# Optimization experiments

Measured on AMD Instinct MI355X. Metric: run time of the kernel, lower is better.

## Reference

```python
import jax, jax.numpy as jnp
import numpy as np

SIGMA = 4.0
KSIZE = 2 * int(4.0 * SIGMA + 0.5) + 1  # 33, as in anomalib's GaussianBlur2d
INPUT_SIZE = (224, 224)
NUM_NEIGHBORS = 9


def avg_pool_4_1_1(x):
    # nn.AvgPool2d(kernel_size=4, stride=1, padding=1), count_include_pad=True -> divide by 16
    s = jax.lax.reduce_window(x, 0.0, jax.lax.add, (1, 1, 4, 4), (1, 1, 1, 1),
                              ((0, 0), (0, 0), (1, 1), (1, 1)))
    return s / 16.0


def gaussian_kernel1d(ksize, sigma):
    x = jnp.arange(ksize, dtype=jnp.float32) - (ksize - 1) / 2.0
    g = jnp.exp(-0.5 * (x / sigma) ** 2)
    return g / jnp.sum(g)


def gaussian_blur(x):
    # separable 33x33 gaussian blur, reflect padding (kornia GaussianBlur2d default)
    k = gaussian_kernel1d(KSIZE, SIGMA)
    pad = KSIZE // 2
    xp = jnp.pad(x, ((0, 0), (0, 0), (pad, pad), (pad, pad)), mode='reflect')
    dn = ('NCHW', 'OIHW', 'NCHW')
    y = jax.lax.conv_general_dilated(xp, k.reshape(1, 1, KSIZE, 1), (1, 1), 'VALID', dimension_numbers=dn)
    y = jax.lax.conv_general_dilated(y, k.reshape(1, 1, 1, KSIZE), (1, 1), 'VALID', dimension_numbers=dn)
    return y


def euclidean_dist(x, y):
    # pairwise L2: x [..., n, d], y [..., m, d] -> [..., n, m]
    x2 = jnp.sum(x * x, axis=-1, keepdims=True)
    y2 = jnp.sum(y * y, axis=-1, keepdims=True)
    d2 = x2 - 2.0 * jnp.matmul(x, jnp.swapaxes(y, -1, -2)) + jnp.swapaxes(y2, -1, -2)
    return jnp.sqrt(jnp.clip(d2, 0.0, None))


def compute_anomaly_score(patch_scores, locations, embedding, memory_bank):
    # PatchCore re-weighting (num_neighbors > 1 branch)
    B, P = patch_scores.shape
    bidx = jnp.arange(B)
    max_patches = jnp.argmax(patch_scores, axis=1)                      # [B]
    feats = embedding.reshape(B, P, -1)[bidx, max_patches]              # [B, C]
    score = patch_scores[bidx, max_patches]                             # [B] s*
    nn_index = locations[bidx, max_patches]                             # [B]
    nn_sample = memory_bank[nn_index]                                   # [B, C]
    d_bank = euclidean_dist(nn_sample, memory_bank)                     # [B, M]
    _, support = jax.lax.top_k(-d_bank, NUM_NEIGHBORS)                  # [B, K] smallest
    support_feats = memory_bank[support]                                # [B, K, C]
    distances = euclidean_dist(feats[:, None, :], support_feats)        # [B, 1, K]
    weights = 1.0 - jnp.exp(score) / jnp.sum(jnp.exp(distances[:, 0, :]), axis=-1)
    return weights * score


def setup_inputs() -> dict:
    key = jax.random.key(0)
    k1, k2, k3 = jax.random.split(key, 3)
    feat_layer2 = jax.random.normal(k1, (8, 512, 28, 28), dtype=jnp.float32)
    feat_layer3 = jax.random.normal(k2, (8, 1024, 14, 14), dtype=jnp.float32)
    memory_bank = jax.random.normal(k3, (32000, 1536), dtype=jnp.float32)
    return {"feat_layer2": feat_layer2, "feat_layer3": feat_layer3, "memory_bank": memory_bank}


def reference(feat_layer2, feat_layer3, memory_bank):
    # feature_pooler = AvgPool2d(4,1,1)
    f2 = avg_pool_4_1_1(feat_layer2)   # [B, 512, 27, 27]
    f3 = avg_pool_4_1_1(feat_layer3)   # [B, 1024, 13, 13]
    B, _, H, W = f2.shape
    # generate_embedding: bilinear upsample layer3 to layer2 size, concat channels
    f3u = jax.image.resize(f3, (B, f3.shape[1], H, W), method='bilinear')
    emb = jnp.concatenate([f2, f3u], axis=1)                            # [B, 1536, 27, 27]
    C = emb.shape[1]
    embedding = jnp.transpose(emb, (0, 2, 3, 1)).reshape(-1, C)         # [B*H*W, C]
    # nearest_neighbors with n_neighbors=1 over the coreset memory bank
    d = euclidean_dist(embedding, memory_bank)                          # [B*H*W, M]
    patch_scores = jnp.min(d, axis=1).reshape(B, -1)
    locations = jnp.argmin(d, axis=1).reshape(B, -1)
    pred_score = compute_anomaly_score(patch_scores, locations, embedding, memory_bank)
    # anomaly map: upsample patch scores to input size + gaussian blur
    pmap = patch_scores.reshape(B, 1, H, W)
    amap = jax.image.resize(pmap, (B, 1, INPUT_SIZE[0], INPUT_SIZE[1]), method='bilinear')
    anomaly_map = gaussian_blur(amap)
    return anomaly_map, pred_score
```

## Files before the change

kernel.cpp:

```cpp
#include <hip/hip_runtime.h>
#include <math.h>

#define NB 8
#define C2 512
#define C3 1024
#define HIN2 28
#define HIN3 14
#define HO2 27
#define HO3 13
#define CC 1536
#define NP (NB*HO2*HO2)
#define NM 32000
#define NKNN 9
#define OH 224
#define AMAP_N (NB*OH*OH)

#define BM 256
#define BN 256
#define BK 64
#define KT (CC/BK)
#define MB_CNT ((NP+BM-1)/BM)
#define NB_CNT (NM/BN)
#define NWG (MB_CNT*NB_CNT)

typedef unsigned long long u64;
typedef unsigned int u32;
typedef __attribute__((ext_vector_type(8))) short bf16x8;
typedef __attribute__((ext_vector_type(4))) float f32x4;

struct GW { float w[33]; };

__device__ __forceinline__ float warp_sum(float v){
  #pragma unroll
  for (int off=32; off; off>>=1) v += __shfl_down(v, off);
  return v;
}

__device__ __forceinline__ ushort f2bf(float f){
  u32 u = __float_as_uint(f);
  u32 r = (u + 0x7FFFu + ((u>>16)&1u)) >> 16;
  return (ushort)r;
}
__device__ __forceinline__ float bf2f(ushort b){
  return __uint_as_float(((u32)b)<<16);
}

#define GLDS(g, l) __builtin_amdgcn_global_load_lds((const __attribute__((address_space(1))) void*)(g), (__attribute__((address_space(3))) void*)(l), 16, 0, 0)
#define WAITVM4() asm volatile("s_waitcnt vmcnt(4)" ::: "memory")
#define WAITVM0() asm volatile("s_waitcnt vmcnt(0)" ::: "memory")
#define WAITLGKM0() asm volatile("s_waitcnt lgkmcnt(0)" ::: "memory")
#define SB0() __builtin_amdgcn_sched_barrier(0)
__device__ __forceinline__ void bar_raw(){
  asm volatile("" ::: "memory");
  __builtin_amdgcn_s_barrier();
  asm volatile("" ::: "memory");
}

__global__ __launch_bounds__(256) void k_avgpool2(const float* __restrict__ in, ushort* __restrict__ embB){
  __shared__ float pl[16*789];
  int b = blockIdx.x >> 5, cg = blockIdx.x & 31;
  const float4* src = (const float4*)(in + ((size_t)b*C2 + cg*16)*(HIN2*HIN2));
  for (int idx = threadIdx.x; idx < 16*196; idx += 256){
    int c = idx/196, p4 = idx - c*196;
    float4 v = src[idx];
    float* d = &pl[c*789 + p4*4];
    d[0]=v.x; d[1]=v.y; d[2]=v.z; d[3]=v.w;
  }
  __syncthreads();
  int c = threadIdx.x & 15, g = threadIdx.x >> 4;
  for (int pos = g; pos < HO2*HO2; pos += 16){
    int i = pos/HO2, j = pos - i*HO2;
    const float* p = &pl[c*789];
    float s = 0.f;
    #pragma unroll
    for (int di=0; di<4; ++di){
      int y = i - 1 + di;
      if ((unsigned)y >= HIN2) continue;
      #pragma unroll
      for (int dj=0; dj<4; ++dj){
        int x = j - 1 + dj;
        if ((unsigned)x < HIN2) s += p[y*HIN2 + x];
      }
    }
    embB[((size_t)((b*HO2 + i)*HO2 + j))*CC + cg*16 + c] = f2bf(s * (1.f/16.f));
  }
}

__global__ __launch_bounds__(256) void k_avgpool3(const float* __restrict__ in, float* __restrict__ f3p){
  __shared__ float pl[64*197];
  int b = blockIdx.x >> 4, cg = blockIdx.x & 15;
  const float4* src = (const float4*)(in + ((size_t)b*C3 + cg*64)*(HIN3*HIN3));
  for (int idx = threadIdx.x; idx < 64*49; idx += 256){
    int c = idx/49, p4 = idx - c*49;
    float4 v = src[idx];
    float* d = &pl[c*197 + p4*4];
    d[0]=v.x; d[1]=v.y; d[2]=v.z; d[3]=v.w;
  }
  __syncthreads();
  int c = threadIdx.x & 63, g = threadIdx.x >> 6;
  for (int pos = g; pos < HO3*HO3; pos += 4){
    int i = pos/HO3, j = pos - i*HO3;
    const float* p = &pl[c*197];
    float s = 0.f;
    #pragma unroll
    for (int di=0; di<4; ++di){
      int y = i - 1 + di;
      if ((unsigned)y >= HIN3) continue;
      #pragma unroll
      for (int dj=0; dj<4; ++dj){
        int x = j - 1 + dj;
        if ((unsigned)x < HIN3) s += p[y*HIN3 + x];
      }
    }
    f3p[((size_t)((b*HO3 + i)*HO3 + j))*C3 + cg*64 + c] = s * (1.f/16.f);
  }
}

__global__ void k_upsample3(const float* __restrict__ f3p, ushort* __restrict__ embB){
  int t = blockIdx.x*256 + threadIdx.x;
  if (t >= NB*HO2*HO2*C3) return;
  int c = t % C3; int r = t / C3;
  int ox = r % HO2; r /= HO2;
  int oy = r % HO2; int b = r / HO2;
  float fy = (oy + 0.5f) * (13.f/27.f) - 0.5f;
  float fx = (ox + 0.5f) * (13.f/27.f) - 0.5f;
  int y0 = (int)floorf(fy); float wy = fy - (float)y0;
  int x0 = (int)floorf(fx); float wx = fx - (float)x0;
  int y0c = min(max(y0,0), HO3-1), y1c = min(max(y0+1,0), HO3-1);
  int x0c = min(max(x0,0), HO3-1), x1c = min(max(x0+1,0), HO3-1);
  const float* base = f3p + (size_t)(b*HO3*HO3)*C3;
  float v00 = base[(size_t)(y0c*HO3 + x0c)*C3 + c];
  float v01 = base[(size_t)(y0c*HO3 + x1c)*C3 + c];
  float v10 = base[(size_t)(y1c*HO3 + x0c)*C3 + c];
  float v11 = base[(size_t)(y1c*HO3 + x1c)*C3 + c];
  float v = (1.f-wy)*((1.f-wx)*v00 + wx*v01) + wy*((1.f-wx)*v10 + wx*v11);
  embB[((size_t)((b*HO2 + oy)*HO2 + ox))*CC + C2 + c] = f2bf(v);
}

__global__ void k_bank_prep(const float* __restrict__ bank, ushort* __restrict__ bankB,
                            float* __restrict__ y2){
  int wave = threadIdx.x >> 6, lane = threadIdx.x & 63;
  int r = blockIdx.x*4 + wave;
  if (r >= NM) return;
  const float4* p = (const float4*)(bank + (size_t)r*CC);
  ushort4* q = (ushort4*)(bankB + (size_t)r*CC);
  float s = 0.f;
  #pragma unroll
  for (int it=0; it<6; ++it){
    float4 v = p[it*64 + lane];
    s += v.x*v.x + v.y*v.y + v.z*v.z + v.w*v.w;
    ushort4 o; o.x = f2bf(v.x); o.y = f2bf(v.y); o.z = f2bf(v.z); o.w = f2bf(v.w);
    q[it*64 + lane] = o;
  }
  s = warp_sum(s);
  if (lane==0) y2[r] = s;
}

__global__ void k_rowsumsq_bf(const ushort* __restrict__ src, float* __restrict__ dst, int rows,
                              u64* __restrict__ packed){
  int wave = threadIdx.x >> 6;
  int lane = threadIdx.x & 63;
  int r = blockIdx.x*4 + wave;
  if (r >= rows) return;
  const uint4* p = (const uint4*)(src + (size_t)r*CC);
  float s = 0.f;
  #pragma unroll
  for (int it=0; it<3; ++it){
    uint4 v = p[it*64 + lane];
    u32 ws_[4] = {v.x, v.y, v.z, v.w};
    #pragma unroll
    for (int q=0;q<4;q++){
      float lo = __uint_as_float(ws_[q]<<16);
      float hi = __uint_as_float(ws_[q]&0xFFFF0000u);
      s += lo*lo + hi*hi;
    }
  }
  s = warp_sum(s);
  if (lane==0){ dst[r] = s; packed[r] = ~0ull; }
}

__global__ __launch_bounds__(512, 2) void k_distmin_mfma(
    const ushort* __restrict__ A, const ushort* __restrict__ B,
    const float* __restrict__ x2, const float* __restrict__ y2,
    u64* __restrict__ packed)
{
  __shared__ ushort smem[4*BM*BK];
  ushort* As0 = smem;
  ushort* Bs0 = smem + BM*BK;
  ushort* As1 = smem + 2*BM*BK;
  ushort* Bs1 = smem + 3*BM*BK;

  const int tid = threadIdx.x;
  const int w   = tid >> 6;
  const int l   = tid & 63;
  const int wr  = w >> 2;
  const int wc  = w & 3;
  const int ccol = l & 15;
  const int cgrp = l >> 4;

  int orig = blockIdx.x;
  const int q8 = NWG/8, r8 = NWG%8;
  int xcd = orig & 7, sidx = orig >> 3;
  int wg = (xcd < r8 ? xcd*(q8+1) : r8*(q8+1) + (xcd-r8)*q8) + sidx;
  const int mb = wg % MB_CNT;
  const int nb = wg / MB_CNT;
  const int m0 = mb * BM;
  const int n0 = nb * BN;

  const int rowin = l >> 3;
  const int scol  = (((l&7) ^ rowin) * 8);
  int chA1[2], chA2[2], chB1[2], chB2[2];
  u32 aO1[2], aO2[2], bO1[2], bO2[2];
  u32 lA1[2], lA2[2], lB1[2], lB2[2];
  #pragma unroll
  for (int c=0;c<2;c++){
    chA1[c] = (w<4) ? (2*w+c) : (8+2*w+c);
    chA2[c] = chA1[c] + 8;
    chB1[c] = (w>>1)*8 + (w&1)*2 + c;
    chB2[c] = chB1[c] + 4;
    aO1[c] = (u32)min(m0 + chA1[c]*8 + rowin, NP-1)*CC + scol;
    aO2[c] = (u32)min(m0 + chA2[c]*8 + rowin, NP-1)*CC + scol;
    bO1[c] = (u32)(n0 + chB1[c]*8 + rowin)*CC + scol;
    bO2[c] = (u32)(n0 + chB2[c]*8 + rowin)*CC + scol;
    lA1[c] = (u32)chA1[c]*1024 + l*16;
    lA2[c] = (u32)chA2[c]*1024 + l*16;
    lB1[c] = (u32)chB1[c]*1024 + l*16;
    lB2[c] = (u32)chB2[c]*1024 + l*16;
  }

  const u32 o0 = (u32)((cgrp ^ (ccol & 7)) * 8);
  u32 aRow[8], bRow[4];
  #pragma unroll
  for (int mi=0;mi<8;mi++) aRow[mi] = (u32)(wr*128 + mi*16 + ccol)*BK;
  #pragma unroll
  for (int ni=0;ni<4;ni++) bRow[ni] = (u32)(wc*64 + ni*16 + ccol)*BK;

  f32x4 acc[8][4];
  #pragma unroll
  for (int mi=0;mi<8;mi++)
    #pragma unroll
    for (int ni=0;ni<4;ni++)
      acc[mi][ni] = (f32x4){0.f,0.f,0.f,0.f};

  bf16x8 rAlo[4][2], rAhi[4][2], rBlo[2][2], rBhi[2][2];

  GLDS(A + aO1[0], (char*)As0 + lA1[0]);
  GLDS(A + aO1[1], (char*)As0 + lA1[1]);
  GLDS(B + bO1[0], (char*)Bs0 + lB1[0]);
  GLDS(B + bO1[1], (char*)Bs0 + lB1[1]);
  GLDS(B + bO2[0], (char*)Bs0 + lB2[0]);
  GLDS(B + bO2[1], (char*)Bs0 + lB2[1]);
  GLDS(A + aO2[0], (char*)As0 + lA2[0]);
  GLDS(A + aO2[1], (char*)As0 + lA2[1]);
  WAITVM4();
  bar_raw();

  const ushort* cA = As0; const ushort* cB = Bs0;
  ushort* nA = As1; ushort* nB = Bs1;

  #pragma unroll 1
  for (int kt=0; kt<KT; ++kt){
    const u32 kk = (u32)(kt+1)*BK;

    #pragma unroll
    for (int mi=0;mi<4;mi++)
      #pragma unroll
      for (int ks=0;ks<2;ks++)
        rAlo[mi][ks] = *(const bf16x8*)&cA[aRow[mi] + (o0 ^ (u32)(ks<<5))];
    #pragma unroll
    for (int ni=0;ni<2;ni++)
      #pragma unroll
      for (int ks=0;ks<2;ks++)
        rBlo[ni][ks] = *(const bf16x8*)&cB[bRow[ni] + (o0 ^ (u32)(ks<<5))];
    GLDS(A + aO1[0] + kk, (char*)nA + lA1[0]);
    GLDS(A + aO1[1] + kk, (char*)nA + lA1[1]);
    bar_raw(); WAITLGKM0(); SB0();
    __builtin_amdgcn_s_setprio(1);
    #pragma unroll
    for (int mi=0;mi<4;mi++)
      #pragma unroll
      for (int ni=0;ni<2;ni++)
        #pragma unroll
        for (int ks=0;ks<2;ks++)
          acc[mi][ni] = __builtin_amdgcn_mfma_f32_16x16x32_bf16(rAlo[mi][ks], rBlo[ni][ks], acc[mi][ni], 0, 0, 0);
    __builtin_amdgcn_s_setprio(0);
    WAITVM4();
    bar_raw();

    #pragma unroll
    for (int ni=0;ni<2;ni++)
      #pragma unroll
      for (int ks=0;ks<2;ks++)
        rBhi[ni][ks] = *(const bf16x8*)&cB[bRow[ni+2] + (o0 ^ (u32)(ks<<5))];
    GLDS(B + bO1[0] + kk, (char*)nB + lB1[0]);
    GLDS(B + bO1[1] + kk, (char*)nB + lB1[1]);
    bar_raw(); WAITLGKM0(); SB0();
    __builtin_amdgcn_s_setprio(1);
    #pragma unroll
    for (int mi=0;mi<4;mi++)
      #pragma unroll
      for (int ni=0;ni<2;ni++)
        #pragma unroll
        for (int ks=0;ks<2;ks++)
          acc[mi][ni+2] = __builtin_amdgcn_mfma_f32_16x16x32_bf16(rAlo[mi][ks], rBhi[ni][ks], acc[mi][ni+2], 0, 0, 0);
    __builtin_amdgcn_s_setprio(0);
    WAITVM4();
    bar_raw();

    #pragma unroll
    for (int mi=0;mi<4;mi++)
      #pragma unroll
      for (int ks=0;ks<2;ks++)
        rAhi[mi][ks] = *(const bf16x8*)&cA[aRow[mi+4] + (o0 ^ (u32)(ks<<5))];
    GLDS(B + bO2[0] + kk, (char*)nB + lB2[0]);
    GLDS(B + bO2[1] + kk, (char*)nB + lB2[1]);
    bar_raw(); WAITLGKM0(); SB0();
    __builtin_amdgcn_s_setprio(1);
    #pragma unroll
    for (int mi=0;mi<4;mi++)
      #pragma unroll
      for (int ni=0;ni<2;ni++)
        #pragma unroll
        for (int ks=0;ks<2;ks++)
          acc[mi+4][ni] = __builtin_amdgcn_mfma_f32_16x16x32_bf16(rAhi[mi][ks], rBlo[ni][ks], acc[mi+4][ni], 0, 0, 0);
    __builtin_amdgcn_s_setprio(0);
    bar_raw();

    GLDS(A + aO2[0] + kk, (char*)nA + lA2[0]);
    GLDS(A + aO2[1] + kk, (char*)nA + lA2[1]);
    bar_raw();
    __builtin_amdgcn_s_setprio(1);
    #pragma unroll
    for (int mi=0;mi<4;mi++)
      #pragma unroll
      for (int ni=0;ni<2;ni++)
        #pragma unroll
        for (int ks=0;ks<2;ks++)
          acc[mi+4][ni+2] = __builtin_amdgcn_mfma_f32_16x16x32_bf16(rAhi[mi][ks], rBhi[ni][ks], acc[mi+4][ni+2], 0, 0, 0);
    __builtin_amdgcn_s_setprio(0);
    WAITVM4();
    bar_raw();

    ushort* t1 = (ushort*)cA; cA = nA; nA = t1;
    ushort* t2 = (ushort*)cB; cB = nB; nB = t2;
  }
  WAITVM0();

  float xv[8][4];
  #pragma unroll
  for (int mi=0;mi<8;mi++)
    #pragma unroll
    for (int r=0;r<4;r++)
      xv[mi][r] = x2[min(m0 + wr*128 + mi*16 + cgrp*4 + r, NP-1)];

  u64 best[8][4];
  #pragma unroll
  for (int mi=0;mi<8;mi++)
    #pragma unroll
    for (int r=0;r<4;r++) best[mi][r] = ~0ull;

  #pragma unroll
  for (int ni=0;ni<4;ni++){
    const int n = n0 + wc*64 + ni*16 + ccol;
    const float yy = y2[n];
    #pragma unroll
    for (int mi=0;mi<8;mi++)
      #pragma unroll
      for (int r=0;r<4;r++){
        float d2 = fmaxf(xv[mi][r] + yy - 2.f*acc[mi][ni][r], 0.f);
        u64 pk = (((u64)__float_as_uint(d2))<<32) | (u32)n;
        if (pk < best[mi][r]) best[mi][r] = pk;
      }
  }

  #pragma unroll
  for (int mi=0;mi<8;mi++)
    #pragma unroll
    for (int r=0;r<4;r++){
      u64 pk = best[mi][r];
      #pragma unroll
      for (int md=1; md<16; md<<=1){
        u64 o = __shfl_xor(pk, md);
        if (o < pk) pk = o;
      }
      const int row = m0 + wr*128 + mi*16 + cgrp*4 + r;
      if (ccol==0 && row < NP) atomicMin(&packed[row], pk);
    }
}

__global__ void k_unpack(const u64* __restrict__ packed, float* __restrict__ patch_d, int* __restrict__ loc){
  int t = blockIdx.x*256 + threadIdx.x;
  if (t < NP){
    u64 v = packed[t];
    patch_d[t] = sqrtf(__uint_as_float((u32)(v>>32)));
    loc[t] = (int)(v & 0xffffffffu);
  }
}

__global__ void k_argmax(const float* __restrict__ patch_d, const int* __restrict__ loc,
                         int* __restrict__ sel_mp, float* __restrict__ sel_score, int* __restrict__ sel_nn){
  int b = blockIdx.x;
  int tid = threadIdx.x;
  __shared__ u64 red[4];
  u64 best = 0;
  for (int p = tid; p < HO2*HO2; p += 256){
    float v = patch_d[b*HO2*HO2 + p];
    u64 pk = (((u64)__float_as_uint(v))<<32) | (u32)(HO2*HO2 - p);
    if (pk > best) best = pk;
  }
  int lane = tid & 63, w = tid >> 6;
  #pragma unroll
  for (int d=32; d; d>>=1){ u64 o = __shfl_down(best, d); if (o > best) best = o; }
  if (lane==0) red[w] = best;
  __syncthreads();
  if (tid==0){
    u64 bb = red[0];
    for (int q=1;q<4;q++) if (red[q] > bb) bb = red[q];
    int p = HO2*HO2 - (int)(bb & 0xffffffffu);
    sel_mp[b] = p;
    sel_score[b] = __uint_as_float((u32)(bb>>32));
    sel_nn[b] = loc[b*HO2*HO2 + p];
  }
}

__device__ __forceinline__ void bf8dec(uint4 v, float* f){
  u32 a[4] = {v.x, v.y, v.z, v.w};
  #pragma unroll
  for (int q=0;q<4;q++){
    f[2*q]   = __uint_as_float(a[q]<<16);
    f[2*q+1] = __uint_as_float(a[q]&0xFFFF0000u);
  }
}

__global__ __launch_bounds__(256) void k_dbank(const ushort* __restrict__ bankB, const float* __restrict__ y2,
    const int* __restrict__ sel_nn, float* __restrict__ d_bank){
  int wave = threadIdx.x >> 6, lane = threadIdx.x & 63;
  int m = blockIdx.x*4 + wave;
  if (m >= NM) return;
  int nn[NB];
  #pragma unroll
  for (int b=0;b<NB;b++) nn[b] = sel_nn[b];
  const uint4* pm = (const uint4*)(bankB + (size_t)m*CC);
  float acc[NB];
  #pragma unroll
  for (int b=0;b<NB;b++) acc[b] = 0.f;
  #pragma unroll
  for (int it=0; it<3; ++it){
    uint4 v = pm[it*64 + lane];
    float vf[8]; bf8dec(v, vf);
    #pragma unroll
    for (int b=0;b<NB;b++){
      uint4 u = ((const uint4*)(bankB + (size_t)nn[b]*CC))[it*64 + lane];
      float uf[8]; bf8dec(u, uf);
      #pragma unroll
      for (int q=0;q<8;q++) acc[b] += vf[q]*uf[q];
    }
  }
  #pragma unroll
  for (int b=0;b<NB;b++){
    float s = warp_sum(acc[b]);
    if (lane==0) d_bank[(size_t)b*NM + m] = fmaxf(y2[nn[b]] + y2[m] - 2.f*s, 0.f);
  }
}

__global__ __launch_bounds__(512) void k_score(const float* __restrict__ d_bank, const float* __restrict__ bank,
    const ushort* __restrict__ embB, const float* __restrict__ x2, const float* __restrict__ y2,
    const int* __restrict__ sel_mp, const float* __restrict__ sel_score, float* __restrict__ out_score){
  int b = blockIdx.x, tid = threadIdx.x;
  __shared__ u64 cand[512*NKNN];
  __shared__ int sel[NKNN];
  __shared__ u64 red[8];
  __shared__ u64 gbest_s;
  __shared__ float fred[8];
  __shared__ float sumexp_s;

  #pragma unroll
  for (int q=0;q<NKNN;q++) cand[tid*NKNN+q] = ~0ull;
  for (int m = tid; m < NM; m += 512){
    float v = d_bank[(size_t)b*NM + m];
    u64 pk = (((u64)__float_as_uint(v))<<32) | (u32)m;
    if (pk < cand[tid*NKNN + NKNN-1]){
      cand[tid*NKNN + NKNN-1] = pk;
      for (int q=NKNN-1; q>0 && cand[tid*NKNN+q] < cand[tid*NKNN+q-1]; --q){
        u64 t = cand[tid*NKNN+q]; cand[tid*NKNN+q] = cand[tid*NKNN+q-1]; cand[tid*NKNN+q-1] = t;
      }
    }
  }
  __syncthreads();
  int lane = tid & 63, w = tid >> 6;
  for (int k=0;k<NKNN;++k){
    u64 mybest = ~0ull;
    #pragma unroll
    for (int q=0;q<NKNN;q++){ u64 v = cand[tid*NKNN+q]; if (v < mybest) mybest = v; }
    u64 rb = mybest;
    #pragma unroll
    for (int d=32; d; d>>=1){ u64 o = __shfl_down(rb, d); if (o < rb) rb = o; }
    if (lane==0) red[w] = rb;
    __syncthreads();
    if (tid==0){
      u64 bb = red[0];
      for (int q=1;q<8;q++) if (red[q] < bb) bb = red[q];
      gbest_s = bb;
      sel[k] = (int)(bb & 0xffffffffu);
    }
    __syncthreads();
    u64 gb = gbest_s;
    #pragma unroll
    for (int q=0;q<NKNN;q++) if (cand[tid*NKNN+q] == gb) cand[tid*NKNN+q] = ~0ull;
    __syncthreads();
  }

  int mp = sel_mp[b];
  const ushort* fv = embB + (size_t)(b*HO2*HO2 + mp)*CC;
  float fx2 = x2[b*HO2*HO2 + mp];
  if (tid==0) sumexp_s = 0.f;
  __syncthreads();
  for (int k=0;k<NKNN;++k){
    const float* sv = bank + (size_t)sel[k]*CC;
    float part = 0.f;
    for (int i = tid; i < CC; i += 512) part += bf2f(fv[i])*sv[i];
    part = warp_sum(part);
    if (lane==0) fred[w] = part;
    __syncthreads();
    if (tid==0){
      float dot = 0.f;
      for (int q=0;q<8;q++) dot += fred[q];
      float d2 = fmaxf(fx2 + y2[sel[k]] - 2.f*dot, 0.f);
      sumexp_s += expf(sqrtf(d2));
    }
    __syncthreads();
  }
  if (tid==0){
    float s = sel_score[b];
    out_score[b] = (1.f - expf(s)/sumexp_s) * s;
  }
}

__global__ void k_maketab(float* __restrict__ T, GW gw){
  int idx = blockIdx.x*256 + threadIdx.x;
  if (idx >= OH*HO2) return;
  int x = idx / HO2, j = idx - x*HO2;
  float s = 0.f;
  #pragma unroll
  for (int k=0;k<33;++k){
    int yy = x + k - 16;
    yy = (yy < 0) ? -yy : yy;
    yy = (yy > OH-1) ? (2*(OH-1) - yy) : yy;
    float fy = (yy + 0.5f) * (27.f/224.f) - 0.5f;
    int y0 = (int)floorf(fy); float wy = fy - (float)y0;
    int j0 = min(max(y0,0), HO2-1), j1 = min(max(y0+1,0), HO2-1);
    float c = ((j==j0)?(1.f-wy):0.f) + ((j==j1)?wy:0.f);
    s += gw.w[k]*c;
  }
  T[idx] = s;
}

__global__ __launch_bounds__(256) void k_amap_fused(const float* __restrict__ patch_d,
    const float* __restrict__ T, float* __restrict__ out){
  __shared__ float Ts[OH*HO2];
  __shared__ float ps[HO2*HO2];
  __shared__ float tmp[HO2*OH];
  int b = blockIdx.x, t = threadIdx.x;
  for (int idx=t; idx<OH*HO2; idx+=256) Ts[idx] = T[idx];
  for (int idx=t; idx<HO2*HO2; idx+=256) ps[idx] = patch_d[b*HO2*HO2+idx];
  __syncthreads();
  for (int idx=t; idx<HO2*OH; idx+=256){
    int i = idx/OH, x = idx - i*OH;
    float s = 0.f;
    #pragma unroll
    for (int j=0;j<HO2;j++) s += ps[i*HO2+j]*Ts[x*HO2+j];
    tmp[i*OH+x] = s;
  }
  __syncthreads();
  for (int idx=t; idx<OH*OH; idx+=256){
    int y = idx/OH, x = idx - y*OH;
    float s = 0.f;
    #pragma unroll
    for (int i=0;i<HO2;i++) s += Ts[y*HO2+i]*tmp[i*OH+x];
    out[(size_t)b*OH*OH + idx] = s;
  }
}

extern "C" void kernel_launch(void* const* d_in, const int* in_sizes, int n_in,
                              void* d_out, int out_size, void* d_ws, size_t ws_size,
                              hipStream_t stream){
  const float* f2   = (const float*)d_in[0];
  const float* f3   = (const float*)d_in[1];
  const float* bank = (const float*)d_in[2];
  float* out = (float*)d_out;

  char* ws = (char*)d_ws;
  size_t off = 0;
  auto alloc = [&](size_t bytes)->char*{ char* p = ws + off; off += (bytes + 255) & ~(size_t)255; return p; };
  ushort* embB    = (ushort*)alloc((size_t)NP*CC*2);
  ushort* bankB   = (ushort*)alloc((size_t)NM*CC*2);
  float* f3p      = (float*)alloc((size_t)NB*HO3*HO3*C3*4);
  float* y2       = (float*)alloc((size_t)NM*4);
  float* x2       = (float*)alloc((size_t)NP*4);
  u64*   packed   = (u64*)  alloc((size_t)NP*8);
  float* patch_d  = (float*)alloc((size_t)NP*4);
  int*   loc      = (int*)  alloc((size_t)NP*4);
  float* d_bank   = (float*)alloc((size_t)NB*NM*4);
  int*   sel_mp   = (int*)  alloc(NB*4);
  float* sel_scr  = (float*)alloc(NB*4);
  int*   sel_nn   = (int*)  alloc(NB*4);
  float* Tmat     = (float*)alloc((size_t)OH*HO2*4);

  GW gw;
  { float s=0.f; for(int i=0;i<33;i++){ float xx=(float)i-16.f; gw.w[i]=expf(-0.5f*(xx/4.f)*(xx/4.f)); s+=gw.w[i]; }
    for(int i=0;i<33;i++) gw.w[i]/=s; }

  k_avgpool2<<<NB*32,256,0,stream>>>(f2, embB);
  k_avgpool3<<<NB*16,256,0,stream>>>(f3, f3p);
  k_upsample3<<<(NB*HO2*HO2*C3+255)/256,256,0,stream>>>(f3p, embB);
  k_bank_prep<<<(NM+3)/4,256,0,stream>>>(bank, bankB, y2);
  k_rowsumsq_bf<<<(NP+3)/4,256,0,stream>>>(embB, x2, NP, packed);
  k_maketab<<<(OH*HO2+255)/256,256,0,stream>>>(Tmat, gw);
  k_distmin_mfma<<<NWG,512,0,stream>>>(embB, bankB, x2, y2, packed);
  k_unpack<<<(NP+255)/256,256,0,stream>>>(packed, patch_d, loc);
  k_argmax<<<NB,256,0,stream>>>(patch_d, loc, sel_mp, sel_scr, sel_nn);
  k_dbank<<<(NM+3)/4,256,0,stream>>>(bankB, y2, sel_nn, d_bank);
  k_score<<<NB,512,0,stream>>>(d_bank, bank, embB, x2, y2, sel_mp, sel_scr, out + AMAP_N);
  k_amap_fused<<<NB,256,0,stream>>>(patch_d, Tmat, out);
}
```

Baseline: 949.6 us.

## Load A fragments directly from global into registers, keep B in LDS

The distance GEMM kernel stops staging the embedding (A) tile through LDS. Each wave now loads its A fragments straight from global memory into registers and prefetches the next K step between MFMA halves. Only the memory-bank (B) tile stays double-buffered in LDS, which halves LDS use and removes several barriers and lgkm waits per K step. The tile order also changes so the N index varies fastest. In exchange, the four column waves fetch the same A rows redundantly from cache with less coalesced per-lane 16-byte loads, and the prefetch on the final step reads past the end of K.

After: 1.784 ms. 1.88x slower.

```diff
diff --git a/kernel.cpp b/kernel.cpp
--- a/kernel.cpp
+++ b/kernel.cpp
@@ -46,9 +46,8 @@
 }
 
 #define GLDS(g, l) __builtin_amdgcn_global_load_lds((const __attribute__((address_space(1))) void*)(g), (__attribute__((address_space(3))) void*)(l), 16, 0, 0)
-#define WAITVM4() asm volatile("s_waitcnt vmcnt(4)" ::: "memory")
+#define WAITVM16() asm volatile("s_waitcnt vmcnt(16)" ::: "memory")
 #define WAITVM0() asm volatile("s_waitcnt vmcnt(0)" ::: "memory")
-#define WAITLGKM0() asm volatile("s_waitcnt lgkmcnt(0)" ::: "memory")
 #define SB0() __builtin_amdgcn_sched_barrier(0)
 __device__ __forceinline__ void bar_raw(){
   asm volatile("" ::: "memory");
@@ -184,11 +183,9 @@
     const float* __restrict__ x2, const float* __restrict__ y2,
     u64* __restrict__ packed)
 {
-  __shared__ ushort smem[4*BM*BK];
-  ushort* As0 = smem;
-  ushort* Bs0 = smem + BM*BK;
-  ushort* As1 = smem + 2*BM*BK;
-  ushort* Bs1 = smem + 3*BM*BK;
+  __shared__ ushort smem[2*BN*BK];
+  ushort* Bs0 = smem;
+  ushort* Bs1 = smem + BN*BK;
 
   const int tid = threadIdx.x;
   const int w   = tid >> 6;
@@ -202,36 +199,28 @@
   const int q8 = NWG/8, r8 = NWG%8;
   int xcd = orig & 7, sidx = orig >> 3;
   int wg = (xcd < r8 ? xcd*(q8+1) : r8*(q8+1) + (xcd-r8)*q8) + sidx;
-  const int mb = wg % MB_CNT;
-  const int nb = wg / MB_CNT;
+  const int nb = wg % NB_CNT;
+  const int mb = wg / NB_CNT;
   const int m0 = mb * BM;
   const int n0 = nb * BN;
 
   const int rowin = l >> 3;
   const int scol  = (((l&7) ^ rowin) * 8);
-  int chA1[2], chA2[2], chB1[2], chB2[2];
-  u32 aO1[2], aO2[2], bO1[2], bO2[2];
-  u32 lA1[2], lA2[2], lB1[2], lB2[2];
-  #pragma unroll
-  for (int c=0;c<2;c++){
-    chA1[c] = (w<4) ? (2*w+c) : (8+2*w+c);
-    chA2[c] = chA1[c] + 8;
-    chB1[c] = (w>>1)*8 + (w&1)*2 + c;
-    chB2[c] = chB1[c] + 4;
-    aO1[c] = (u32)min(m0 + chA1[c]*8 + rowin, NP-1)*CC + scol;
-    aO2[c] = (u32)min(m0 + chA2[c]*8 + rowin, NP-1)*CC + scol;
-    bO1[c] = (u32)(n0 + chB1[c]*8 + rowin)*CC + scol;
-    bO2[c] = (u32)(n0 + chB2[c]*8 + rowin)*CC + scol;
-    lA1[c] = (u32)chA1[c]*1024 + l*16;
-    lA2[c] = (u32)chA2[c]*1024 + l*16;
-    lB1[c] = (u32)chB1[c]*1024 + l*16;
-    lB2[c] = (u32)chB2[c]*1024 + l*16;
-  }
+  u32 bOff[4]; u32 lOff[4];
+  #pragma unroll
+  for (int c=0;c<4;c++){
+    int chunk = w*4 + c;
+    bOff[c] = (u32)(n0 + chunk*8 + rowin)*CC + scol;
+    lOff[c] = (u32)chunk*1024 + l*16;
+  }
+
+  u32 aOff[8];
+  #pragma unroll
+  for (int mi=0;mi<8;mi++)
+    aOff[mi] = (u32)min(m0 + wr*128 + mi*16 + ccol, NP-1)*CC + cgrp*8;
 
   const u32 o0 = (u32)((cgrp ^ (ccol & 7)) * 8);
-  u32 aRow[8], bRow[4];
-  #pragma unroll
-  for (int mi=0;mi<8;mi++) aRow[mi] = (u32)(wr*128 + mi*16 + ccol)*BK;
+  u32 bRow[4];
   #pragma unroll
   for (int ni=0;ni<4;ni++) bRow[ni] = (u32)(wc*64 + ni*16 + ccol)*BK;
 
@@ -242,107 +231,72 @@
     for (int ni=0;ni<4;ni++)
       acc[mi][ni] = (f32x4){0.f,0.f,0.f,0.f};
 
-  bf16x8 rAlo[4][2], rAhi[4][2], rBlo[2][2], rBhi[2][2];
-
-  GLDS(A + aO1[0], (char*)As0 + lA1[0]);
-  GLDS(A + aO1[1], (char*)As0 + lA1[1]);
-  GLDS(B + bO1[0], (char*)Bs0 + lB1[0]);
-  GLDS(B + bO1[1], (char*)Bs0 + lB1[1]);
-  GLDS(B + bO2[0], (char*)Bs0 + lB2[0]);
-  GLDS(B + bO2[1], (char*)Bs0 + lB2[1]);
-  GLDS(A + aO2[0], (char*)As0 + lA2[0]);
-  GLDS(A + aO2[1], (char*)As0 + lA2[1]);
-  WAITVM4();
-  bar_raw();
-
-  const ushort* cA = As0; const ushort* cB = Bs0;
-  ushort* nA = As1; ushort* nB = Bs1;
+  bf16x8 aF[8][2], bF[4][2];
+
+  #pragma unroll
+  for (int c=0;c<4;c++) GLDS(B + bOff[c], (char*)Bs0 + lOff[c]);
+  #pragma unroll
+  for (int mi=0;mi<8;mi++)
+    #pragma unroll
+    for (int ks=0;ks<2;ks++)
+      aF[mi][ks] = *(const bf16x8*)(A + aOff[mi] + ks*32);
+  #pragma unroll
+  for (int mi=0;mi<8;mi++) aOff[mi] += 64;
+  WAITVM0(); bar_raw(); SB0();
+
+  const ushort* cB = Bs0; ushort* nB = Bs1;
 
   #pragma unroll 1
   for (int kt=0; kt<KT; ++kt){
-    const u32 kk = (u32)(kt+1)*BK;
-
+    #pragma unroll
+    for (int ni=0;ni<4;ni++)
+      #pragma unroll
+      for (int ks=0;ks<2;ks++)
+        bF[ni][ks] = *(const bf16x8*)&cB[bRow[ni] + (o0 ^ (u32)(ks<<5))];
+
+    #pragma unroll
+    for (int c=0;c<4;c++) bOff[c] += 64;
+    #pragma unroll
+    for (int c=0;c<4;c++) GLDS(B + bOff[c], (char*)nB + lOff[c]);
+    SB0();
+
+    __builtin_amdgcn_s_setprio(1);
     #pragma unroll
     for (int mi=0;mi<4;mi++)
       #pragma unroll
-      for (int ks=0;ks<2;ks++)
-        rAlo[mi][ks] = *(const bf16x8*)&cA[aRow[mi] + (o0 ^ (u32)(ks<<5))];
-    #pragma unroll
-    for (int ni=0;ni<2;ni++)
-      #pragma unroll
-      for (int ks=0;ks<2;ks++)
-        rBlo[ni][ks] = *(const bf16x8*)&cB[bRow[ni] + (o0 ^ (u32)(ks<<5))];
-    GLDS(A + aO1[0] + kk, (char*)nA + lA1[0]);
-    GLDS(A + aO1[1] + kk, (char*)nA + lA1[1]);
-    bar_raw(); WAITLGKM0(); SB0();
-    __builtin_amdgcn_s_setprio(1);
-    #pragma unroll
-    for (int mi=0;mi<4;mi++)
-      #pragma unroll
-      for (int ni=0;ni<2;ni++)
+      for (int ni=0;ni<4;ni++)
         #pragma unroll
         for (int ks=0;ks<2;ks++)
-          acc[mi][ni] = __builtin_amdgcn_mfma_f32_16x16x32_bf16(rAlo[mi][ks], rBlo[ni][ks], acc[mi][ni], 0, 0, 0);
+          acc[mi][ni] = __builtin_amdgcn_mfma_f32_16x16x32_bf16(aF[mi][ks], bF[ni][ks], acc[mi][ni], 0, 0, 0);
     __builtin_amdgcn_s_setprio(0);
-    WAITVM4();
-    bar_raw();
-
-    #pragma unroll
-    for (int ni=0;ni<2;ni++)
+
+    #pragma unroll
+    for (int mi=0;mi<4;mi++)
       #pragma unroll
       for (int ks=0;ks<2;ks++)
-        rBhi[ni][ks] = *(const bf16x8*)&cB[bRow[ni+2] + (o0 ^ (u32)(ks<<5))];
-    GLDS(B + bO1[0] + kk, (char*)nB + lB1[0]);
-    GLDS(B + bO1[1] + kk, (char*)nB + lB1[1]);
-    bar_raw(); WAITLGKM0(); SB0();
+        aF[mi][ks] = *(const bf16x8*)(A + aOff[mi] + ks*32);
+
     __builtin_amdgcn_s_setprio(1);
     #pragma unroll
-    for (int mi=0;mi<4;mi++)
-      #pragma unroll
-      for (int ni=0;ni<2;ni++)
+    for (int mi=4;mi<8;mi++)
+      #pragma unroll
+      for (int ni=0;ni<4;ni++)
         #pragma unroll
         for (int ks=0;ks<2;ks++)
-          acc[mi][ni+2] = __builtin_amdgcn_mfma_f32_16x16x32_bf16(rAlo[mi][ks], rBhi[ni][ks], acc[mi][ni+2], 0, 0, 0);
+          acc[mi][ni] = __builtin_amdgcn_mfma_f32_16x16x32_bf16(aF[mi][ks], bF[ni][ks], acc[mi][ni], 0, 0, 0);
     __builtin_amdgcn_s_setprio(0);
-    WAITVM4();
-    bar_raw();
-
-    #pragma unroll
-    for (int mi=0;mi<4;mi++)
+
+    #pragma unroll
+    for (int mi=4;mi<8;mi++)
       #pragma unroll
       for (int ks=0;ks<2;ks++)
-        rAhi[mi][ks] = *(const bf16x8*)&cA[aRow[mi+4] + (o0 ^ (u32)(ks<<5))];
-    GLDS(B + bO2[0] + kk, (char*)nB + lB2[0]);
-    GLDS(B + bO2[1] + kk, (char*)nB + lB2[1]);
-    bar_raw(); WAITLGKM0(); SB0();
-    __builtin_amdgcn_s_setprio(1);
-    #pragma unroll
-    for (int mi=0;mi<4;mi++)
-      #pragma unroll
-      for (int ni=0;ni<2;ni++)
-        #pragma unroll
-        for (int ks=0;ks<2;ks++)
-          acc[mi+4][ni] = __builtin_amdgcn_mfma_f32_16x16x32_bf16(rAhi[mi][ks], rBlo[ni][ks], acc[mi+4][ni], 0, 0, 0);
-    __builtin_amdgcn_s_setprio(0);
-    bar_raw();
-
-    GLDS(A + aO2[0] + kk, (char*)nA + lA2[0]);
-    GLDS(A + aO2[1] + kk, (char*)nA + lA2[1]);
-    bar_raw();
-    __builtin_amdgcn_s_setprio(1);
-    #pragma unroll
-    for (int mi=0;mi<4;mi++)
-      #pragma unroll
-      for (int ni=0;ni<2;ni++)
-        #pragma unroll
-        for (int ks=0;ks<2;ks++)
-          acc[mi+4][ni+2] = __builtin_amdgcn_mfma_f32_16x16x32_bf16(rAhi[mi][ks], rBhi[ni][ks], acc[mi+4][ni+2], 0, 0, 0);
-    __builtin_amdgcn_s_setprio(0);
-    WAITVM4();
-    bar_raw();
-
-    ushort* t1 = (ushort*)cA; cA = nA; nA = t1;
-    ushort* t2 = (ushort*)cB; cB = nB; nB = t2;
+        aF[mi][ks] = *(const bf16x8*)(A + aOff[mi] + ks*32);
+    #pragma unroll
+    for (int mi=0;mi<8;mi++) aOff[mi] += 64;
+
+    WAITVM16();
+    bar_raw(); SB0();
+    ushort* t = (ushort*)cB; cB = nB; nB = t;
   }
   WAITVM0();
 
```

## Prefetch next LDS fragments during MFMA phases and drop explicit lgkm waits

Applied to the files above, without the earlier changes.

Restructures the GEMM main loop schedule so each of the four MFMA phases overlaps with the LDS-to-register read of the next phase's fragments, including the next k-tile's A-lo and B-lo from the freshly loaded buffer. The prologue is rewritten to load only the first half of the tile, preload the first fragments, and then issue the remaining global-to-LDS loads. Barriers now come before the global_load_lds issue with vmcnt(2) waits, and the explicit lgkmcnt(0) waits are removed. The aim is to hide LDS read latency behind matrix ops. It relies on subtle counter and barrier ordering to avoid buffer races, and may change register pressure.

Result: no change. 938.7 us (-1.2%).

```diff
diff --git a/kernel.cpp b/kernel.cpp
--- a/kernel.cpp
+++ b/kernel.cpp
@@ -46,9 +46,8 @@
 }
 
 #define GLDS(g, l) __builtin_amdgcn_global_load_lds((const __attribute__((address_space(1))) void*)(g), (__attribute__((address_space(3))) void*)(l), 16, 0, 0)
-#define WAITVM4() asm volatile("s_waitcnt vmcnt(4)" ::: "memory")
+#define WAITVM2() asm volatile("s_waitcnt vmcnt(2)" ::: "memory")
 #define WAITVM0() asm volatile("s_waitcnt vmcnt(0)" ::: "memory")
-#define WAITLGKM0() asm volatile("s_waitcnt lgkmcnt(0)" ::: "memory")
 #define SB0() __builtin_amdgcn_sched_barrier(0)
 __device__ __forceinline__ void bar_raw(){
   asm volatile("" ::: "memory");
@@ -244,16 +243,25 @@
 
   bf16x8 rAlo[4][2], rAhi[4][2], rBlo[2][2], rBhi[2][2];
 
-  GLDS(A + aO1[0], (char*)As0 + lA1[0]);
-  GLDS(A + aO1[1], (char*)As0 + lA1[1]);
-  GLDS(B + bO1[0], (char*)Bs0 + lB1[0]);
-  GLDS(B + bO1[1], (char*)Bs0 + lB1[1]);
-  GLDS(B + bO2[0], (char*)Bs0 + lB2[0]);
-  GLDS(B + bO2[1], (char*)Bs0 + lB2[1]);
-  GLDS(A + aO2[0], (char*)As0 + lA2[0]);
-  GLDS(A + aO2[1], (char*)As0 + lA2[1]);
-  WAITVM4();
-  bar_raw();
+  #pragma unroll
+  for (int c=0;c<2;c++) GLDS(A + aO1[c], (char*)As0 + lA1[c]);
+  #pragma unroll
+  for (int c=0;c<2;c++) GLDS(B + bO1[c], (char*)Bs0 + lB1[c]);
+  WAITVM0(); bar_raw();
+  #pragma unroll
+  for (int mi=0;mi<4;mi++)
+    #pragma unroll
+    for (int ks=0;ks<2;ks++)
+      rAlo[mi][ks] = *(const bf16x8*)&As0[aRow[mi] + (o0 ^ (u32)(ks<<5))];
+  #pragma unroll
+  for (int ni=0;ni<2;ni++)
+    #pragma unroll
+    for (int ks=0;ks<2;ks++)
+      rBlo[ni][ks] = *(const bf16x8*)&Bs0[bRow[ni] + (o0 ^ (u32)(ks<<5))];
+  #pragma unroll
+  for (int c=0;c<2;c++) GLDS(B + bO2[c], (char*)Bs0 + lB2[c]);
+  #pragma unroll
+  for (int c=0;c<2;c++) GLDS(A + aO2[c], (char*)As0 + lA2[c]);
 
   const ushort* cA = As0; const ushort* cB = Bs0;
   ushort* nA = As1; ushort* nB = Bs1;
@@ -262,19 +270,14 @@
   for (int kt=0; kt<KT; ++kt){
     const u32 kk = (u32)(kt+1)*BK;
 
-    #pragma unroll
-    for (int mi=0;mi<4;mi++)
-      #pragma unroll
-      for (int ks=0;ks<2;ks++)
-        rAlo[mi][ks] = *(const bf16x8*)&cA[aRow[mi] + (o0 ^ (u32)(ks<<5))];
-    #pragma unroll
-    for (int ni=0;ni<2;ni++)
-      #pragma unroll
-      for (int ks=0;ks<2;ks++)
-        rBlo[ni][ks] = *(const bf16x8*)&cB[bRow[ni] + (o0 ^ (u32)(ks<<5))];
+    WAITVM2(); bar_raw(); SB0();
     GLDS(A + aO1[0] + kk, (char*)nA + lA1[0]);
     GLDS(A + aO1[1] + kk, (char*)nA + lA1[1]);
-    bar_raw(); WAITLGKM0(); SB0();
+    #pragma unroll
+    for (int ni=0;ni<2;ni++)
+      #pragma unroll
+      for (int ks=0;ks<2;ks++)
+        rBhi[ni][ks] = *(const bf16x8*)&cB[bRow[ni+2] + (o0 ^ (u32)(ks<<5))];
     __builtin_amdgcn_s_setprio(1);
     #pragma unroll
     for (int mi=0;mi<4;mi++)
@@ -284,17 +287,15 @@
         for (int ks=0;ks<2;ks++)
           acc[mi][ni] = __builtin_amdgcn_mfma_f32_16x16x32_bf16(rAlo[mi][ks], rBlo[ni][ks], acc[mi][ni], 0, 0, 0);
     __builtin_amdgcn_s_setprio(0);
-    WAITVM4();
-    bar_raw();
-
-    #pragma unroll
-    for (int ni=0;ni<2;ni++)
-      #pragma unroll
-      for (int ks=0;ks<2;ks++)
-        rBhi[ni][ks] = *(const bf16x8*)&cB[bRow[ni+2] + (o0 ^ (u32)(ks<<5))];
+
+    WAITVM2(); bar_raw(); SB0();
     GLDS(B + bO1[0] + kk, (char*)nB + lB1[0]);
     GLDS(B + bO1[1] + kk, (char*)nB + lB1[1]);
-    bar_raw(); WAITLGKM0(); SB0();
+    #pragma unroll
+    for (int mi=0;mi<4;mi++)
+      #pragma unroll
+      for (int ks=0;ks<2;ks++)
+        rAhi[mi][ks] = *(const bf16x8*)&cA[aRow[mi+4] + (o0 ^ (u32)(ks<<5))];
     __builtin_amdgcn_s_setprio(1);
     #pragma unroll
     for (int mi=0;mi<4;mi++)
@@ -304,17 +305,15 @@
         for (int ks=0;ks<2;ks++)
           acc[mi][ni+2] = __builtin_amdgcn_mfma_f32_16x16x32_bf16(rAlo[mi][ks], rBhi[ni][ks], acc[mi][ni+2], 0, 0, 0);
     __builtin_amdgcn_s_setprio(0);
-    WAITVM4();
-    bar_raw();
-
-    #pragma unroll
-    for (int mi=0;mi<4;mi++)
-      #pragma unroll
-      for (int ks=0;ks<2;ks++)
-        rAhi[mi][ks] = *(const bf16x8*)&cA[aRow[mi+4] + (o0 ^ (u32)(ks<<5))];
+
+    WAITVM2(); bar_raw(); SB0();
     GLDS(B + bO2[0] + kk, (char*)nB + lB2[0]);
     GLDS(B + bO2[1] + kk, (char*)nB + lB2[1]);
-    bar_raw(); WAITLGKM0(); SB0();
+    #pragma unroll
+    for (int mi=0;mi<4;mi++)
+      #pragma unroll
+      for (int ks=0;ks<2;ks++)
+        rAlo[mi][ks] = *(const bf16x8*)&((const ushort*)nA)[aRow[mi] + (o0 ^ (u32)(ks<<5))];
     __builtin_amdgcn_s_setprio(1);
     #pragma unroll
     for (int mi=0;mi<4;mi++)
@@ -324,11 +323,15 @@
         for (int ks=0;ks<2;ks++)
           acc[mi+4][ni] = __builtin_amdgcn_mfma_f32_16x16x32_bf16(rAhi[mi][ks], rBlo[ni][ks], acc[mi+4][ni], 0, 0, 0);
     __builtin_amdgcn_s_setprio(0);
-    bar_raw();
-
+
+    WAITVM2(); bar_raw(); SB0();
     GLDS(A + aO2[0] + kk, (char*)nA + lA2[0]);
     GLDS(A + aO2[1] + kk, (char*)nA + lA2[1]);
-    bar_raw();
+    #pragma unroll
+    for (int ni=0;ni<2;ni++)
+      #pragma unroll
+      for (int ks=0;ks<2;ks++)
+        rBlo[ni][ks] = *(const bf16x8*)&((const ushort*)nB)[bRow[ni] + (o0 ^ (u32)(ks<<5))];
     __builtin_amdgcn_s_setprio(1);
     #pragma unroll
     for (int mi=0;mi<4;mi++)
@@ -338,8 +341,6 @@
         for (int ks=0;ks<2;ks++)
           acc[mi+4][ni+2] = __builtin_amdgcn_mfma_f32_16x16x32_bf16(rAhi[mi][ks], rBhi[ni][ks], acc[mi+4][ni+2], 0, 0, 0);
     __builtin_amdgcn_s_setprio(0);
-    WAITVM4();
-    bar_raw();
 
     ushort* t1 = (ushort*)cA; cA = nA; nA = t1;
     ushort* t2 = (ushort*)cB; cB = nB; nB = t2;
```
